# Optimization experiments

Measured on AMD Instinct MI355X. Metric: run time of the kernel, lower is better.

The kernel has to match this reference:

```python
import jax, jax.numpy as jnp
import numpy as np

BIN_SIZE = 128
DIST_MULT = 0.1
CLIP_LOW = 0.0
LN_EPS = 1e-6


def setup_inputs() -> dict:
    key = jax.random.key(0)
    ks = jax.random.split(key, 16)
    B, N, F = 8, 12800, 256
    D, H = 128, 256          # distance_dim, hidden_dim
    MAX_BINS = 200
    s = lambda k, shape: jax.random.normal(k, shape, dtype=jnp.float32) * 0.05
    return {
        "x": jax.random.normal(ks[0], (B, N, F), dtype=jnp.float32),
        "msk": jnp.ones((B, N), dtype=bool),
        "rotations": jax.random.normal(ks[1], (D, MAX_BINS // 2), dtype=jnp.float32),
        "ln_gamma": jnp.ones((F,), dtype=jnp.float32),
        "ln_beta": jnp.zeros((F,), dtype=jnp.float32),
        "w0": s(ks[2], (F, H)), "b0": jnp.zeros((H,), jnp.float32),
        "w1": s(ks[3], (H, H)), "b1": jnp.zeros((H,), jnp.float32),
        "w2": s(ks[4], (H, D)), "b2": jnp.zeros((D,), jnp.float32),
        "W_t": s(ks[5], (F, F)), "b_t": jnp.zeros((F,), jnp.float32),
        "W_h": s(ks[6], (F, F)),
        "theta": s(ks[7], (F, F)),
    }


def _forward(x, msk, rotations, ln_gamma, ln_beta, w0, b0, w1, b1, w2, b2,
             W_t, b_t, W_h, theta):
    B, N, F = x.shape
    n_bins = N // BIN_SIZE

    # LayerNormalization(axis=-1, epsilon=1e-6)
    mu = jnp.mean(x, axis=-1, keepdims=True)
    var = jnp.var(x, axis=-1, keepdims=True)
    xn = (x - mu) * jax.lax.rsqrt(var + LN_EPS) * ln_gamma + ln_beta

    # ffn_dist: two elu hidden layers + linear output to distance_dim
    h = jax.nn.elu(xn @ w0 + b0)
    h = jax.nn.elu(h @ w1 + b1)
    x_dist = h @ w2 + b2                                   # [B, N, D]

    # LSH binning: project, argmax over signed projections, argsort into bins
    mul = x_dist @ rotations[:, : n_bins // 2]             # [B, N, n_bins/2]
    cmul = jnp.concatenate([mul, -mul], axis=-1)           # [B, N, n_bins]
    bin_idx = jnp.argmax(cmul, axis=-1) + jnp.where(~msk, n_bins - 1, 0)
    bins_split = jnp.argsort(bin_idx, axis=-1).reshape(B, n_bins, BIN_SIZE)
    flat = bins_split.reshape(B, N)

    def take(a):  # gather with batch_dims=1, then split into bins
        return jnp.take_along_axis(a, flat[..., None], axis=1).reshape(
            B, n_bins, BIN_SIZE, a.shape[-1])

    x_msg_b = take(x_dist)                                 # [B, nb, bs, D]
    x_feat_b = take(xn)                                    # [B, nb, bs, F]
    msk_b = take(msk.astype(x.dtype)[..., None])           # [B, nb, bs, 1]

    # NodePairGaussianKernel on each bin
    na = jnp.sum(x_msg_b * x_msg_b, axis=-1)               # [B, nb, bs]
    d2 = (na[..., :, None] - 2.0 * jnp.einsum('bnif,bnjf->bnij', x_msg_b, x_msg_b)
          + na[..., None, :])
    dm = jnp.exp(-DIST_MULT * jnp.sqrt(jnp.maximum(d2, 1e-6)))
    dm = jnp.clip(dm, CLIP_LOW, 1.0)
    m = msk_b[..., 0]
    dm = dm * m[..., :, None] * m[..., None, :]            # [B, nb, bs, bs]

    # GHConvDense message passing (normalize_degrees=True, elu)
    in_deg = jnp.clip(jnp.sum(jnp.abs(dm), axis=-1), 0.0, 1000.0)
    norm = ((in_deg + 1e-6) ** -0.5)[..., None] * msk_b    # [B, nb, bs, 1]
    xm = x_feat_b * msk_b
    f_hom = (xm @ theta) * msk_b
    f_hom = jnp.einsum('bnij,bnjf->bnif', dm, f_hom * norm) * norm
    f_het = xm @ W_h
    gate = jax.nn.sigmoid(x_feat_b @ W_t + b_t)
    out = jax.nn.elu(gate * f_hom + (1.0 - gate) * f_het) * msk_b

    # reverse_lsh: scatter binned points back to original order
    pts = out.reshape(B, N, F)
    enc = jnp.zeros_like(pts).at[jnp.arange(B)[:, None], flat].set(pts)
    return enc


def reference(x, msk, rotations, ln_gamma, ln_beta, w0, b0, w1, b1, w2, b2,
              W_t, b_t, W_h, theta):
    return _forward(x, msk, rotations, ln_gamma, ln_beta, w0, b0, w1, b1,
                    w2, b2, W_t, b_t, W_h, theta)
```

## Files before the change

### kernel.cpp

```cpp
#include <hip/hip_runtime.h>


#define Bc   8
#define Nc   12800
#define Fc   256
#define Dc   128
#define NBINS 100
#define NBH  50
#define NPB  64
#define SPLT2 16384
#define TIE_TAU 1.0e-3f
#define FLAG_CAP 16384
#define WS_NEED 133062784ULL

typedef __attribute__((ext_vector_type(8))) short short8v;
typedef __attribute__((ext_vector_type(8))) _Float16 half8v;
typedef __attribute__((ext_vector_type(4))) _Float16 half4v;
typedef __attribute__((ext_vector_type(4))) float f32x4;

__device__ __forceinline__ float eluf(float v) { return v > 0.f ? v : __expf(v) - 1.f; }
__device__ __forceinline__ unsigned short f2bf(float f) {
  unsigned u = __float_as_uint(f);
  unsigned r = (u + 0x7FFFu + ((u >> 16) & 1u)) >> 16;
  return (unsigned short)r;
}
__device__ __forceinline__ float bf2f(unsigned short h) {
  return __uint_as_float((unsigned)h << 16);
}
__device__ __forceinline__ void split2(float v, _Float16 h[2]) {
  h[0] = (_Float16)v;
  h[1] = (_Float16)((v - (float)h[0]) * 2048.f);
}
#define C1 (1.f/2048.f)

__global__ void k0_prep(const float* __restrict__ theta, const float* __restrict__ Wh,
                        const float* __restrict__ Wt, const float* __restrict__ w0,
                        const float* __restrict__ w1, const float* __restrict__ w2,
                        const float* __restrict__ rot,
                        unsigned short* __restrict__ wcat, _Float16* __restrict__ w0s,
                        _Float16* __restrict__ w1s, _Float16* __restrict__ w2s,
                        _Float16* __restrict__ rots, int* __restrict__ flag_cnt)
{
  const int k = blockIdx.x, n = threadIdx.x;
  if (k == 0 && n == 0) *flag_cnt = 0;
  for (int nn = n; nn < 768; nn += 256) {
    const int sel = nn >> 8, f = nn & 255;
    const float* W = sel == 0 ? theta : (sel == 1 ? Wh : Wt);
    wcat[(size_t)nn*256 + k] = f2bf(W[k*256 + f]);
  }
  _Float16 h[2];
  split2(w0[k*256 + n], h);
#pragma unroll
  for (int s = 0; s < 2; ++s) w0s[s*65536 + n*256 + k] = h[s];
  split2(w1[k*256 + n], h);
#pragma unroll
  for (int s = 0; s < 2; ++s) w1s[s*65536 + n*256 + k] = h[s];
  if (n < 128) {
    split2(w2[k*128 + n], h);
#pragma unroll
    for (int s = 0; s < 2; ++s) w2s[s*32768 + n*256 + k] = h[s];
  }
  if (k < 128 && n < 112) {
    const float v = (n < NBINS) ? rot[k*100 + n] : 0.f;
    split2(v, h);
#pragma unroll
    for (int s = 0; s < 2; ++s) rots[s*14336 + n*128 + k] = h[s];
  }
}

template<int RT, int NT, int KS, int NSTR>
__device__ __forceinline__ void gemm3(const _Float16* __restrict__ sAb,
    const _Float16* __restrict__ B, int ldb, int bsplit, int n0, int lr, int lk,
    f32x4 aM[RT][NT], f32x4 aC1[RT][NT])
{
#pragma unroll
  for (int ks = 0; ks < KS; ++ks) {
    half8v a[2][RT], b[2][NT];
#pragma unroll
    for (int s = 0; s < 2; ++s) {
#pragma unroll
      for (int rt = 0; rt < RT; ++rt)
        a[s][rt] = *(const half8v*)&sAb[s*SPLT2 + (ks*4 + lk)*(NPB*8) + (rt*16 + lr)*8];
#pragma unroll
      for (int nt = 0; nt < NT; ++nt)
        b[s][nt] = *(const half8v*)&B[s*bsplit + (n0 + nt*NSTR + lr)*ldb + ks*32 + lk*8];
    }
#pragma unroll
    for (int rt = 0; rt < RT; ++rt)
#pragma unroll
      for (int nt = 0; nt < NT; ++nt) {
        aM[rt][nt]  = __builtin_amdgcn_mfma_f32_16x16x32_f16(a[0][rt], b[0][nt], aM[rt][nt], 0,0,0);
        aC1[rt][nt] = __builtin_amdgcn_mfma_f32_16x16x32_f16(a[0][rt], b[1][nt], aC1[rt][nt],0,0,0);
        aC1[rt][nt] = __builtin_amdgcn_mfma_f32_16x16x32_f16(a[1][rt], b[0][nt], aC1[rt][nt],0,0,0);
      }
  }
}

__global__ __launch_bounds__(512, 2) void k1_mfma(
    const float* __restrict__ x, const float* __restrict__ gamma, const float* __restrict__ beta,
    const _Float16* __restrict__ w0s, const _Float16* __restrict__ w1s,
    const _Float16* __restrict__ w2s, const _Float16* __restrict__ rots,
    const float* __restrict__ b0, const float* __restrict__ b1, const float* __restrict__ b2,
    unsigned short* __restrict__ xn_out, unsigned short* __restrict__ xd_out,
    int* __restrict__ bin_out, int* __restrict__ flag_cnt, int* __restrict__ flag_list)
{
  __shared__ __align__(16) _Float16 sA4[2*SPLT2];

  const int t = threadIdx.x;
  const int w = t >> 6, l = t & 63;
  const int lr = l & 15, lk = l >> 4;
  const int pt0 = blockIdx.x * NPB;

  {
    const int r = t >> 3, c8 = t & 7;
    const float* xr = x + (size_t)(pt0 + r)*Fc + c8*32;
    float4 xv[8];
    float s1 = 0.f, s2 = 0.f;
#pragma unroll
    for (int i = 0; i < 8; ++i) {
      xv[i] = *(const float4*)&xr[i*4];
      s1 += xv[i].x + xv[i].y + xv[i].z + xv[i].w;
      s2 += xv[i].x*xv[i].x + xv[i].y*xv[i].y + xv[i].z*xv[i].z + xv[i].w*xv[i].w;
    }
    s1 += __shfl_xor(s1, 1); s2 += __shfl_xor(s2, 1);
    s1 += __shfl_xor(s1, 2); s2 += __shfl_xor(s2, 2);
    s1 += __shfl_xor(s1, 4); s2 += __shfl_xor(s2, 4);
    const float mu = s1 * (1.f/256.f);
    const float var = s2 * (1.f/256.f) - mu*mu;
    const float rs = 1.f / sqrtf(var + 1e-6f);
#pragma unroll
    for (int i = 0; i < 8; ++i) {
      const int c = c8*32 + i*4;
      const float4 g  = *(const float4*)&gamma[c];
      const float4 be = *(const float4*)&beta[c];
      float v[4] = { (xv[i].x-mu)*rs*g.x + be.x, (xv[i].y-mu)*rs*g.y + be.y,
                     (xv[i].z-mu)*rs*g.z + be.z, (xv[i].w-mu)*rs*g.w + be.w };
      ushort4 ov; _Float16 h[4][2];
#pragma unroll
      for (int e = 0; e < 4; ++e) split2(v[e], h[e]);
      ov.x = f2bf(v[0]); ov.y = f2bf(v[1]); ov.z = f2bf(v[2]); ov.w = f2bf(v[3]);
      *(ushort4*)&xn_out[(size_t)(pt0 + r)*Fc + c] = ov;
      const int off = (c >> 3)*(NPB*8) + r*8 + (c & 7);
#pragma unroll
      for (int s = 0; s < 2; ++s) {
        half4v hv; hv[0]=h[0][s]; hv[1]=h[1][s]; hv[2]=h[2][s]; hv[3]=h[3][s];
        *(half4v*)&sA4[s*SPLT2 + off] = hv;
      }
    }
  }
  __syncthreads();

#pragma unroll 1
  for (int layer = 0; layer < 2; ++layer) {
    const _Float16* Bw = layer ? w1s : w0s;
    const float*    bb = layer ? b1  : b0;
    f32x4 aM[4][2], aC1[4][2];
#pragma unroll
    for (int rt = 0; rt < 4; ++rt)
#pragma unroll
      for (int nt = 0; nt < 2; ++nt) {
        aM[rt][nt] = (f32x4){0,0,0,0}; aC1[rt][nt] = (f32x4){0,0,0,0};
      }
    gemm3<4,2,8,16>(sA4, Bw, 256, 65536, w*32, lr, lk, aM, aC1);
    float vals[4][2][4];
#pragma unroll
    for (int nt = 0; nt < 2; ++nt) {
      const float bias = bb[w*32 + nt*16 + lr];
#pragma unroll
      for (int rt = 0; rt < 4; ++rt)
#pragma unroll
        for (int rr = 0; rr < 4; ++rr)
          vals[rt][nt][rr] = eluf(aM[rt][nt][rr] + aC1[rt][nt][rr]*C1 + bias);
    }
    __syncthreads();
#pragma unroll
    for (int nt = 0; nt < 2; ++nt) {
      const int col = w*32 + nt*16 + lr;
      const int base = (col >> 3)*(NPB*8) + (col & 7);
#pragma unroll
      for (int rt = 0; rt < 4; ++rt)
#pragma unroll
        for (int rr = 0; rr < 4; ++rr) {
          const int row = rt*16 + lk*4 + rr;
          _Float16 h[2]; split2(vals[rt][nt][rr], h);
          const int off = base + row*8;
          sA4[off] = h[0]; sA4[SPLT2 + off] = h[1];
        }
    }
    __syncthreads();
  }

  {
    f32x4 aM[4][1], aC1[4][1];
#pragma unroll
    for (int rt = 0; rt < 4; ++rt) { aM[rt][0] = (f32x4){0,0,0,0}; aC1[rt][0] = (f32x4){0,0,0,0}; }
    gemm3<4,1,8,16>(sA4, w2s, 256, 32768, w*16, lr, lk, aM, aC1);
    float vals[4][4];
    const int col = w*16 + lr;
    const float bias = b2[col];
#pragma unroll
    for (int rt = 0; rt < 4; ++rt)
#pragma unroll
      for (int rr = 0; rr < 4; ++rr) {
        const float v = aM[rt][0][rr] + aC1[rt][0][rr]*C1 + bias;
        vals[rt][rr] = v;
        xd_out[(size_t)(pt0 + rt*16 + lk*4 + rr)*Dc + col] = f2bf(v);
      }
    __syncthreads();
    {
      const int base = (col >> 3)*(NPB*8) + (col & 7);
#pragma unroll
      for (int rt = 0; rt < 4; ++rt)
#pragma unroll
        for (int rr = 0; rr < 4; ++rr) {
          const int row = rt*16 + lk*4 + rr;
          _Float16 h[2]; split2(vals[rt][rr], h);
          const int off = base + row*8;
          sA4[off] = h[0]; sA4[SPLT2 + off] = h[1];
        }
    }
    __syncthreads();
  }

  {
    float pv[4][4];
    if (w < 7) {
      f32x4 aM[4][1], aC1[4][1];
#pragma unroll
      for (int rt = 0; rt < 4; ++rt) { aM[rt][0] = (f32x4){0,0,0,0}; aC1[rt][0] = (f32x4){0,0,0,0}; }
      gemm3<4,1,4,16>(sA4, rots, 128, 14336, w*16, lr, lk, aM, aC1);
#pragma unroll
      for (int rt = 0; rt < 4; ++rt)
#pragma unroll
        for (int rr = 0; rr < 4; ++rr)
          pv[rt][rr] = aM[rt][0][rr] + aC1[rt][0][rr]*C1;
    }
    float* sMul = (float*)sA4;
    __syncthreads();
    if (w < 7) {
#pragma unroll
      for (int rt = 0; rt < 4; ++rt)
#pragma unroll
        for (int rr = 0; rr < 4; ++rr)
          sMul[(rt*16 + lk*4 + rr)*116 + w*16 + lr] = pv[rt][rr];
    }
    __syncthreads();
    if (t < NPB) {
      float best = -3.0e38f, second = -3.0e38f; int bi = 0;
      for (int j = 0; j < NBINS; ++j) {
        const float v = (j < NBH) ? sMul[t*116 + j] : -sMul[t*116 + (j - NBH)];
        if (v > best) { second = best; best = v; bi = j; }
        else if (v > second) second = v;
      }
      bin_out[pt0 + t] = bi;
      if (best - second < TIE_TAU) {
        const int slot = atomicAdd(flag_cnt, 1);
        if (slot < FLAG_CAP) flag_list[slot] = pt0 + t;
      }
    }
  }
}

__global__ __launch_bounds__(256) void k1b_repair(
    const float* __restrict__ x, const float* __restrict__ gamma, const float* __restrict__ beta,
    const float* __restrict__ w0, const float* __restrict__ b0,
    const float* __restrict__ w1, const float* __restrict__ b1,
    const float* __restrict__ w2, const float* __restrict__ b2,
    const float* __restrict__ rot,
    const int* __restrict__ flag_cnt, const int* __restrict__ flag_list,
    int* __restrict__ bin_out)
{
  const int n = min(*flag_cnt, FLAG_CAP);
  __shared__ float s0[256], s1[256], rs1[4], rs2[4];
  const int t = threadIdx.x;

  for (int it = blockIdx.x; it < n; it += gridDim.x) {
    const int p = flag_list[it];
    const float xv = x[(size_t)p*Fc + t];
    float a1 = xv, a2 = xv*xv;
#pragma unroll
    for (int o = 1; o < 64; o <<= 1) { a1 += __shfl_xor(a1, o); a2 += __shfl_xor(a2, o); }
    if ((t & 63) == 0) { rs1[t>>6] = a1; rs2[t>>6] = a2; }
    __syncthreads();
    const float S1 = rs1[0]+rs1[1]+rs1[2]+rs1[3];
    const float S2 = rs2[0]+rs2[1]+rs2[2]+rs2[3];
    const float mu = S1 * (1.f/256.f);
    const float var = S2 * (1.f/256.f) - mu*mu;
    const float rsv = 1.f / sqrtf(var + 1e-6f);
    s0[t] = (xv - mu) * rsv * gamma[t] + beta[t];
    __syncthreads();
    float acc = 0.f;
    for (int k = 0; k < 256; ++k) acc += s0[k] * w0[k*256 + t];
    const float h0v = eluf(acc + b0[t]);
    __syncthreads(); s1[t] = h0v; __syncthreads();
    acc = 0.f;
    for (int k = 0; k < 256; ++k) acc += s1[k] * w1[k*256 + t];
    const float h1v = eluf(acc + b1[t]);
    __syncthreads(); s0[t] = h1v; __syncthreads();
    if (t < 128) {
      acc = 0.f;
      for (int k = 0; k < 256; ++k) acc += s0[k] * w2[k*128 + t];
      s1[t] = acc + b2[t];
    }
    __syncthreads();
    if (t < NBINS) {
      float m = 0.f;
      for (int d = 0; d < 128; ++d) m += s1[d] * rot[d*100 + t];
      s0[t] = m;
    }
    __syncthreads();
    if (t == 0) {
      float best = -3.0e38f; int bi = 0;
      for (int j = 0; j < NBINS; ++j) {
        const float v = (j < NBH) ? s0[j] : -s0[j - NBH];
        if (v > best) { best = v; bi = j; }
      }
      bin_out[p] = bi;
    }
    __syncthreads();
  }
}

__global__ __launch_bounds__(256) void k2_sort(const int* __restrict__ bin_idx,
                                               int* __restrict__ flat)
{
  __shared__ unsigned int hist[NBINS][256];
  __shared__ unsigned int off[NBINS];
  const int b = blockIdx.x, t = threadIdx.x;
  for (int i = t; i < NBINS*256; i += 256) ((unsigned int*)hist)[i] = 0u;
  __syncthreads();
  const int* bi = bin_idx + b*Nc;
  const int start = t * 50;
  for (int i = 0; i < 50; ++i) hist[bi[start+i]][t]++;
  __syncthreads();
  for (int bb = t; bb < NBINS; bb += 256) {
    unsigned run = 0;
    for (int q = 0; q < 256; ++q) { const unsigned v = hist[bb][q]; hist[bb][q] = run; run += v; }
    off[bb] = run;
  }
  __syncthreads();
  if (t == 0) {
    unsigned run = 0;
    for (int q = 0; q < NBINS; ++q) { const unsigned v = off[q]; off[q] = run; run += v; }
  }
  __syncthreads();
  int* fo = flat + b*Nc;
  for (int i = 0; i < 50; ++i) {
    const int idx = start + i;
    const int bb = bi[idx];
    fo[off[bb] + hist[bb][t]++] = idx;
  }
}

__global__ __launch_bounds__(256) void k1g_hg(
    const unsigned short* __restrict__ xn, const unsigned short* __restrict__ wcat,
    const float* __restrict__ bt, float* __restrict__ out,
    unsigned short* __restrict__ gatebuf)
{
  __shared__ __align__(16) unsigned short sX[32*256];
  const int t = threadIdx.x;
  const int w = t >> 6, l = t & 63;
  const int lr = l & 15, lk = l >> 4;
  const int pt0 = blockIdx.x * 32;

  {
    const int r = t >> 3, c8 = t & 7;
    const unsigned short* src = xn + (size_t)(pt0 + r)*Fc + c8*32;
#pragma unroll
    for (int i = 0; i < 4; ++i) {
      const int c = c8*32 + i*8;
      *(short8v*)&sX[(c >> 3)*256 + r*8] = *(const short8v*)(src + i*8);
    }
  }
  __syncthreads();

#pragma unroll 1
  for (int cs = 0; cs < 4; ++cs) {
    const int f0 = w*64 + cs*16;
    f32x4 hacc[2], gacc[2];
#pragma unroll
    for (int rt = 0; rt < 2; ++rt) { hacc[rt] = (f32x4){0,0,0,0}; gacc[rt] = (f32x4){0,0,0,0}; }
    const unsigned short* bh = wcat + (size_t)(256 + f0 + lr)*256 + lk*8;
    const unsigned short* bg = wcat + (size_t)(512 + f0 + lr)*256 + lk*8;
#pragma unroll
    for (int ks = 0; ks < 8; ++ks) {
      short8v a0 = *(const short8v*)&sX[(ks*4 + lk)*256 + (lr)*8];
      short8v a1 = *(const short8v*)&sX[(ks*4 + lk)*256 + (16 + lr)*8];
      short8v bhv = *(const short8v*)(bh + ks*32);
      short8v bgv = *(const short8v*)(bg + ks*32);
      hacc[0] = __builtin_amdgcn_mfma_f32_16x16x32_bf16(a0, bhv, hacc[0], 0, 0, 0);
      hacc[1] = __builtin_amdgcn_mfma_f32_16x16x32_bf16(a1, bhv, hacc[1], 0, 0, 0);
      gacc[0] = __builtin_amdgcn_mfma_f32_16x16x32_bf16(a0, bgv, gacc[0], 0, 0, 0);
      gacc[1] = __builtin_amdgcn_mfma_f32_16x16x32_bf16(a1, bgv, gacc[1], 0, 0, 0);
    }
    const int f = f0 + lr;
    const float btf = bt[f];
#pragma unroll
    for (int rt = 0; rt < 2; ++rt)
#pragma unroll
      for (int rr = 0; rr < 4; ++rr) {
        const int p = pt0 + rt*16 + lk*4 + rr;
        const float g = 1.f / (1.f + __expf(-(gacc[rt][rr] + btf)));
        out[(size_t)p*Fc + f] = (1.f - g) * hacc[rt][rr];
        gatebuf[(size_t)p*Fc + f] = f2bf(g);
      }
  }
}

#define SXD 136

__global__ __launch_bounds__(512, 2) void k3_hoist(
    const unsigned short* __restrict__ xn, const unsigned short* __restrict__ xd,
    const int* __restrict__ flat, const unsigned short* __restrict__ wcat,
    const unsigned short* __restrict__ gatebuf, float* __restrict__ out)
{
  __shared__ __align__(16) unsigned short s_xd[128*SXD];
  __shared__ __align__(16) unsigned short s_dm[128*SXD];
  __shared__ __align__(16) unsigned short s_gt[32*SXD];
  __shared__ int   s_idx[128];
  __shared__ float s_na[128];
  __shared__ float s_norm[128];

  const int t = threadIdx.x;
  const int l = t & 63, w = t >> 6;
  const int lr = l & 15, lk = l >> 4;
  const int b = blockIdx.x / NBINS, bin = blockIdx.x % NBINS;
  const int base = b * Nc;

  if (t < 128) s_idx[t] = flat[base + bin*128 + t];
  __syncthreads();

  {
    const int r0 = t >> 4, c = t & 15;
    for (int r = r0; r < 128; r += 32) {
      const unsigned short* src = xd + (size_t)(base + s_idx[r])*Dc + c*8;
      *(short8v*)&s_xd[r*SXD + c*8] = *(const short8v*)src;
    }
  }
  __syncthreads();
  if (t < 128) {
    float s = 0.f;
    for (int c = 0; c < 16; ++c) {
      short8v v = *(short8v*)&s_xd[t*SXD + c*8];
#pragma unroll
      for (int e = 0; e < 8; ++e) { const float f = bf2f((unsigned short)v[e]); s += f*f; }
    }
    s_na[t] = s;
  }
  __syncthreads();

  {
    short8v a[4];
    const int arow = w*16 + lr;
#pragma unroll
    for (int kg = 0; kg < 4; ++kg)
      a[kg] = *(short8v*)&s_xd[arow*SXD + kg*32 + lk*8];
#pragma unroll 1
    for (int tj = 0; tj < 8; ++tj) {
      const int brow = tj*16 + lr;
      f32x4 acc = {0.f, 0.f, 0.f, 0.f};
#pragma unroll
      for (int kg = 0; kg < 4; ++kg) {
        short8v bv = *(short8v*)&s_xd[brow*SXD + kg*32 + lk*8];
        acc = __builtin_amdgcn_mfma_f32_16x16x32_bf16(a[kg], bv, acc, 0, 0, 0);
      }
      const int jj = tj*16 + lr;
      const float naj = s_na[jj];
#pragma unroll
      for (int r = 0; r < 4; ++r) {
        const int ii = w*16 + lk*4 + r;
        const float d2 = s_na[ii] + naj - 2.f*acc[r];
        s_dm[ii*SXD + jj] = f2bf(__expf(-0.1f * sqrtf(fmaxf(d2, 1e-6f))));
      }
    }
  }
  __syncthreads();
  if (t < 128) {
    float s = 0.f;
    for (int c = 0; c < 16; ++c) {
      short8v v = *(short8v*)&s_dm[t*SXD + c*8];
#pragma unroll
      for (int e = 0; e < 8; ++e) s += bf2f((unsigned short)v[e]);
    }
    s = fminf(fmaxf(s, 0.f), 1000.f);
    s_norm[t] = 1.f / sqrtf(s + 1e-6f);
  }
  __syncthreads();

  const size_t xrow = (size_t)(base + s_idx[w*16 + lr]) * Fc;

#pragma unroll 1
  for (int ch = 0; ch < 8; ++ch) {
    const int f0 = ch * 32;
    short8v A[8];
#pragma unroll
    for (int kg = 0; kg < 8; ++kg)
      A[kg] = *(const short8v*)&xn[xrow + kg*32 + lk*8];
#pragma unroll
    for (int tf = 0; tf < 2; ++tf) {
      const int f = f0 + tf*16 + lr;
      const unsigned short* bp = wcat + (size_t)f*256 + lk*8;
      f32x4 tacc = {0.f,0.f,0.f,0.f};
#pragma unroll
      for (int kg = 0; kg < 8; ++kg) {
        short8v bv = *(const short8v*)(bp + kg*32);
        tacc = __builtin_amdgcn_mfma_f32_16x16x32_bf16(A[kg], bv, tacc, 0, 0, 0);
      }
#pragma unroll
      for (int r = 0; r < 4; ++r) {
        const int j = w*16 + lk*4 + r;
        s_gt[(tf*16 + lr)*SXD + j] = f2bf(tacc[r] * s_norm[j]);
      }
    }
    __syncthreads();
    {
      const int irow = w*16 + lr;
#pragma unroll
      for (int tf = 0; tf < 2; ++tf) {
        const int f = f0 + tf*16 + lr;
        f32x4 facc = {0.f, 0.f, 0.f, 0.f};
#pragma unroll
        for (int kg = 0; kg < 4; ++kg) {
          short8v ad  = *(short8v*)&s_dm[irow*SXD + kg*32 + lk*8];
          short8v bgt = *(short8v*)&s_gt[(tf*16 + lr)*SXD + kg*32 + lk*8];
          facc = __builtin_amdgcn_mfma_f32_16x16x32_bf16(ad, bgt, facc, 0, 0, 0);
        }
#pragma unroll
        for (int r = 0; r < 4; ++r) {
          const int i = w*16 + lk*4 + r;
          const size_t orow = (size_t)(base + s_idx[i]) * Fc + f;
          const float fh = facc[r] * s_norm[i];
          const float g  = bf2f(gatebuf[orow]);
          const float partial = out[orow];
          out[orow] = eluf(g * fh + partial);
        }
      }
    }
    __syncthreads();
  }
}

__global__ __launch_bounds__(512, 2) void k3_bins(
    const unsigned short* __restrict__ xn, const unsigned short* __restrict__ xd,
    const int* __restrict__ flat, const unsigned short* __restrict__ wcat,
    const float* __restrict__ bt, float* __restrict__ out)
{
  __shared__ __align__(16) unsigned short s_buf[128*SXD];
  __shared__ __align__(16) unsigned short s_gt[32*SXD];
  __shared__ int   s_idx[128];
  __shared__ float s_na[128];
  __shared__ float s_norm[128];

  const int t = threadIdx.x;
  const int l = t & 63, w = t >> 6;
  const int lr = l & 15, lk = l >> 4;
  const int b = blockIdx.x / NBINS, bin = blockIdx.x % NBINS;
  const int base = b * Nc;

  if (t < 128) s_idx[t] = flat[base + bin*128 + t];
  __syncthreads();
  {
    const int r0 = t >> 4, c = t & 15;
    for (int r = r0; r < 128; r += 32) {
      const unsigned short* src = xd + (size_t)(base + s_idx[r])*Dc + c*8;
      *(short8v*)&s_buf[r*SXD + c*8] = *(const short8v*)src;
    }
  }
  __syncthreads();
  if (t < 128) {
    float s = 0.f;
    for (int c = 0; c < 16; ++c) {
      short8v v = *(short8v*)&s_buf[t*SXD + c*8];
#pragma unroll
      for (int e = 0; e < 8; ++e) { const float f = bf2f((unsigned short)v[e]); s += f*f; }
    }
    s_na[t] = s;
  }
  __syncthreads();
  {
    f32x4 dot[8];
    short8v a[4];
    const int arow = w*16 + lr;
#pragma unroll
    for (int kg = 0; kg < 4; ++kg)
      a[kg] = *(short8v*)&s_buf[arow*SXD + kg*32 + lk*8];
#pragma unroll
    for (int tj = 0; tj < 8; ++tj) {
      const int brow = tj*16 + lr;
      f32x4 acc = {0.f, 0.f, 0.f, 0.f};
#pragma unroll
      for (int kg = 0; kg < 4; ++kg) {
        short8v bv = *(short8v*)&s_buf[brow*SXD + kg*32 + lk*8];
        acc = __builtin_amdgcn_mfma_f32_16x16x32_bf16(a[kg], bv, acc, 0, 0, 0);
      }
      dot[tj] = acc;
    }
    __syncthreads();
#pragma unroll
    for (int tj = 0; tj < 8; ++tj) {
      const int jj = tj*16 + lr;
      const float naj = s_na[jj];
#pragma unroll
      for (int r = 0; r < 4; ++r) {
        const int ii = w*16 + lk*4 + r;
        const float d2 = s_na[ii] + naj - 2.f*dot[tj][r];
        s_buf[ii*SXD + jj] = f2bf(__expf(-0.1f * sqrtf(fmaxf(d2, 1e-6f))));
      }
    }
  }
  __syncthreads();
  if (t < 128) {
    float s = 0.f;
    for (int c = 0; c < 16; ++c) {
      short8v v = *(short8v*)&s_buf[t*SXD + c*8];
#pragma unroll
      for (int e = 0; e < 8; ++e) s += bf2f((unsigned short)v[e]);
    }
    s = fminf(fmaxf(s, 0.f), 1000.f);
    s_norm[t] = 1.f / sqrtf(s + 1e-6f);
  }
  __syncthreads();

  const size_t xrow = (size_t)(base + s_idx[w*16 + lr]) * Fc;
#pragma unroll 1
  for (int ch = 0; ch < 8; ++ch) {
    const int f0 = ch * 32;
    float hg_h[2][4], hg_g[2][4];
    short8v A[8];
#pragma unroll
    for (int kg = 0; kg < 8; ++kg)
      A[kg] = *(const short8v*)&xn[xrow + kg*32 + lk*8];
#pragma unroll
    for (int tf = 0; tf < 2; ++tf) {
      const int f = f0 + tf*16 + lr;
      const unsigned short* bp = wcat + (size_t)f*256 + lk*8;
      const unsigned short* bh = wcat + (size_t)(256 + f)*256 + lk*8;
      const unsigned short* bg = wcat + (size_t)(512 + f)*256 + lk*8;
      f32x4 tacc = {0.f,0.f,0.f,0.f}, hacc = {0.f,0.f,0.f,0.f}, gacc = {0.f,0.f,0.f,0.f};
#pragma unroll
      for (int kg = 0; kg < 8; ++kg) {
        short8v bv = *(const short8v*)(bp + kg*32);
        tacc = __builtin_amdgcn_mfma_f32_16x16x32_bf16(A[kg], bv, tacc, 0, 0, 0);
        short8v hv = *(const short8v*)(bh + kg*32);
        hacc = __builtin_amdgcn_mfma_f32_16x16x32_bf16(A[kg], hv, hacc, 0, 0, 0);
        short8v gv = *(const short8v*)(bg + kg*32);
        gacc = __builtin_amdgcn_mfma_f32_16x16x32_bf16(A[kg], gv, gacc, 0, 0, 0);
      }
#pragma unroll
      for (int r = 0; r < 4; ++r) {
        const int j = w*16 + lk*4 + r;
        s_gt[(tf*16 + lr)*SXD + j] = f2bf(tacc[r] * s_norm[j]);
        hg_h[tf][r] = hacc[r];
        hg_g[tf][r] = gacc[r];
      }
    }
    __syncthreads();
    {
      const int irow = w*16 + lr;
#pragma unroll
      for (int tf = 0; tf < 2; ++tf) {
        const int f = f0 + tf*16 + lr;
        f32x4 facc = {0.f, 0.f, 0.f, 0.f};
#pragma unroll
        for (int kg = 0; kg < 4; ++kg) {
          short8v ad  = *(short8v*)&s_buf[irow*SXD + kg*32 + lk*8];
          short8v bgt = *(short8v*)&s_gt[(tf*16 + lr)*SXD + kg*32 + lk*8];
          facc = __builtin_amdgcn_mfma_f32_16x16x32_bf16(ad, bgt, facc, 0, 0, 0);
        }
        const float btf = bt[f];
#pragma unroll
        for (int r = 0; r < 4; ++r) {
          const int i = w*16 + lk*4 + r;
          const float fh = facc[r] * s_norm[i];
          const float g  = 1.f / (1.f + __expf(-(hg_g[tf][r] + btf)));
          const float val = g * fh + (1.f - g) * hg_h[tf][r];
          out[(size_t)(base + s_idx[i])*Fc + f] = eluf(val);
        }
      }
    }
    __syncthreads();
  }
}

extern "C" void kernel_launch(void* const* d_in, const int* in_sizes, int n_in,
                              void* d_out, int out_size, void* d_ws, size_t ws_size,
                              hipStream_t stream)
{
  const float* x     = (const float*)d_in[0];
  const float* rot   = (const float*)d_in[2];
  const float* gamma = (const float*)d_in[3];
  const float* beta  = (const float*)d_in[4];
  const float* w0    = (const float*)d_in[5];
  const float* b0    = (const float*)d_in[6];
  const float* w1    = (const float*)d_in[7];
  const float* b1    = (const float*)d_in[8];
  const float* w2    = (const float*)d_in[9];
  const float* b2    = (const float*)d_in[10];
  const float* Wt    = (const float*)d_in[11];
  const float* bt    = (const float*)d_in[12];
  const float* Wh    = (const float*)d_in[13];
  const float* theta = (const float*)d_in[14];
  float* out = (float*)d_out;

  char* ws = (char*)d_ws;
  unsigned short* xn   = (unsigned short*)ws;
  unsigned short* xd   = (unsigned short*)(ws + 52428800);
  int* binv            = (int*)(ws + 78643200);
  int* flat            = (int*)(ws + 79052800);
  unsigned short* wcat = (unsigned short*)(ws + 79462400);
  _Float16* w0s        = (_Float16*)(ws + 79855616);
  _Float16* w1s        = (_Float16*)(ws + 80117760);
  _Float16* w2s        = (_Float16*)(ws + 80379904);
  _Float16* rots       = (_Float16*)(ws + 80510976);
  int* fcnt            = (int*)(ws + 80568320);
  int* flist           = (int*)(ws + 80568448);
  unsigned short* gate = (unsigned short*)(ws + 80633984);

  const bool hoist = (ws_size >= WS_NEED);

  k0_prep<<<dim3(256), dim3(256), 0, stream>>>(theta, Wh, Wt, w0, w1, w2, rot,
                                               wcat, w0s, w1s, w2s, rots, fcnt);
  k1_mfma<<<dim3((Bc*Nc)/NPB), dim3(512), 0, stream>>>(
      x, gamma, beta, w0s, w1s, w2s, rots, b0, b1, b2, xn, xd, binv, fcnt, flist);
  k1b_repair<<<dim3(2048), dim3(256), 0, stream>>>(
      x, gamma, beta, w0, b0, w1, b1, w2, b2, rot, fcnt, flist, binv);
  k2_sort<<<dim3(Bc), dim3(256), 0, stream>>>(binv, flat);
  if (hoist) {
    k1g_hg<<<dim3((Bc*Nc)/32), dim3(256), 0, stream>>>(xn, wcat, bt, out, gate);
    k3_hoist<<<dim3(Bc*NBINS), dim3(512), 0, stream>>>(
        xn, xd, flat, wcat, gate, out);
  } else {
    k3_bins<<<dim3(Bc*NBINS), dim3(512), 0, stream>>>(
        xn, xd, flat, wcat, bt, out);
  }
}
```

Baseline: 578.3 us.

## Hoist theta projection into unbinned gate/het kernel, store bf16 intermediate

```diff
diff --git a/kernel.cpp b/kernel.cpp
--- a/kernel.cpp
+++ b/kernel.cpp
@@ -11,7 +11,8 @@
 #define SPLT2 16384
 #define TIE_TAU 1.0e-3f
 #define FLAG_CAP 16384
-#define WS_NEED 133062784ULL
+#define WS_NEED1 133062784ULL
+#define WS_NEED2 185491584ULL
 
 typedef __attribute__((ext_vector_type(8))) short short8v;
 typedef __attribute__((ext_vector_type(8))) _Float16 half8v;
@@ -352,6 +353,68 @@
   }
 }
 
+__global__ __launch_bounds__(256) void k1g_hg3(
+    const unsigned short* __restrict__ xn, const unsigned short* __restrict__ wcat,
+    const float* __restrict__ bt, float* __restrict__ out,
+    unsigned short* __restrict__ gatebuf, unsigned short* __restrict__ gtall)
+{
+  __shared__ __align__(16) unsigned short sX[32*256];
+  const int t = threadIdx.x;
+  const int w = t >> 6, l = t & 63;
+  const int lr = l & 15, lk = l >> 4;
+  const int pt0 = blockIdx.x * 32;
+
+  {
+    const int r = t >> 3, c8 = t & 7;
+    const unsigned short* src = xn + (size_t)(pt0 + r)*Fc + c8*32;
+#pragma unroll
+    for (int i = 0; i < 4; ++i) {
+      const int c = c8*32 + i*8;
+      *(short8v*)&sX[(c >> 3)*256 + r*8] = *(const short8v*)(src + i*8);
+    }
+  }
+  __syncthreads();
+
+#pragma unroll 1
+  for (int cs = 0; cs < 4; ++cs) {
+    const int f0 = w*64 + cs*16;
+    f32x4 hacc[2], gacc[2], tacc[2];
+#pragma unroll
+    for (int rt = 0; rt < 2; ++rt) {
+      hacc[rt] = (f32x4){0,0,0,0}; gacc[rt] = (f32x4){0,0,0,0}; tacc[rt] = (f32x4){0,0,0,0};
+    }
+    const unsigned short* bp = wcat + (size_t)(f0 + lr)*256 + lk*8;
+    const unsigned short* bh = wcat + (size_t)(256 + f0 + lr)*256 + lk*8;
+    const unsigned short* bg = wcat + (size_t)(512 + f0 + lr)*256 + lk*8;
+#pragma unroll
+    for (int ks = 0; ks < 8; ++ks) {
+      short8v a0 = *(const short8v*)&sX[(ks*4 + lk)*256 + (lr)*8];
+      short8v a1 = *(const short8v*)&sX[(ks*4 + lk)*256 + (16 + lr)*8];
+      short8v btv = *(const short8v*)(bp + ks*32);
+      short8v bhv = *(const short8v*)(bh + ks*32);
+      short8v bgv = *(const short8v*)(bg + ks*32);
+      tacc[0] = __builtin_amdgcn_mfma_f32_16x16x32_bf16(a0, btv, tacc[0], 0, 0, 0);
+      tacc[1] = __builtin_amdgcn_mfma_f32_16x16x32_bf16(a1, btv, tacc[1], 0, 0, 0);
+      hacc[0] = __builtin_amdgcn_mfma_f32_16x16x32_bf16(a0, bhv, hacc[0], 0, 0, 0);
+      hacc[1] = __builtin_amdgcn_mfma_f32_16x16x32_bf16(a1, bhv, hacc[1], 0, 0, 0);
+      gacc[0] = __builtin_amdgcn_mfma_f32_16x16x32_bf16(a0, bgv, gacc[0], 0, 0, 0);
+      gacc[1] = __builtin_amdgcn_mfma_f32_16x16x32_bf16(a1, bgv, gacc[1], 0, 0, 0);
+    }
+    const int f = f0 + lr;
+    const float btf = bt[f];
+#pragma unroll
+    for (int rt = 0; rt < 2; ++rt)
+#pragma unroll
+      for (int rr = 0; rr < 4; ++rr) {
+        const int p = pt0 + rt*16 + lk*4 + rr;
+        const float g = 1.f / (1.f + __expf(-(gacc[rt][rr] + btf)));
+        out[(size_t)p*Fc + f] = (1.f - g) * hacc[rt][rr];
+        gatebuf[(size_t)p*Fc + f] = f2bf(g);
+        gtall[(size_t)p*Fc + f] = f2bf(tacc[rt][rr]);
+      }
+  }
+}
+
 __global__ __launch_bounds__(256) void k1g_hg(
     const unsigned short* __restrict__ xn, const unsigned short* __restrict__ wcat,
     const float* __restrict__ bt, float* __restrict__ out,
@@ -409,9 +472,9 @@
 
 #define SXD 136
 
-__global__ __launch_bounds__(512, 2) void k3_hoist(
-    const unsigned short* __restrict__ xn, const unsigned short* __restrict__ xd,
-    const int* __restrict__ flat, const unsigned short* __restrict__ wcat,
+__global__ __launch_bounds__(512, 2) void k3_hoist2(
+    const unsigned short* __restrict__ xd, const int* __restrict__ flat,
+    const unsigned short* __restrict__ gtall,
     const unsigned short* __restrict__ gatebuf, float* __restrict__ out)
 {
   __shared__ __align__(16) unsigned short s_xd[128*SXD];
@@ -487,8 +550,122 @@
   }
   __syncthreads();
 
+#pragma unroll 1
+  for (int ch = 0; ch < 8; ++ch) {
+    const int f0 = ch * 32;
+    {
+      const int r = t >> 2, cc = (t & 3) * 8;
+      short8v v = *(const short8v*)&gtall[(size_t)(base + s_idx[r])*Fc + f0 + cc];
+      const float nr = s_norm[r];
+#pragma unroll
+      for (int e = 0; e < 8; ++e)
+        s_gt[(cc + e)*SXD + r] = f2bf(bf2f((unsigned short)v[e]) * nr);
+    }
+    __syncthreads();
+    {
+      const int irow = w*16 + lr;
+#pragma unroll
+      for (int tf = 0; tf < 2; ++tf) {
+        const int f = f0 + tf*16 + lr;
+        f32x4 facc = {0.f, 0.f, 0.f, 0.f};
+#pragma unroll
+        for (int kg = 0; kg < 4; ++kg) {
+          short8v ad  = *(short8v*)&s_dm[irow*SXD + kg*32 + lk*8];
+          short8v bgt = *(short8v*)&s_gt[(tf*16 + lr)*SXD + kg*32 + lk*8];
+          facc = __builtin_amdgcn_mfma_f32_16x16x32_bf16(ad, bgt, facc, 0, 0, 0);
+        }
+#pragma unroll
+        for (int r = 0; r < 4; ++r) {
+          const int i = w*16 + lk*4 + r;
+          const size_t orow = (size_t)(base + s_idx[i]) * Fc + f;
+          const float fh = facc[r] * s_norm[i];
+          const float g  = bf2f(gatebuf[orow]);
+          const float partial = out[orow];
+          out[orow] = eluf(g * fh + partial);
+        }
+      }
+    }
+    __syncthreads();
+  }
+}
+
+__global__ __launch_bounds__(512, 2) void k3_hoist(
+    const unsigned short* __restrict__ xn, const unsigned short* __restrict__ xd,
+    const int* __restrict__ flat, const unsigned short* __restrict__ wcat,
+    const unsigned short* __restrict__ gatebuf, float* __restrict__ out)
+{
+  __shared__ __align__(16) unsigned short s_xd[128*SXD];
+  __shared__ __align__(16) unsigned short s_dm[128*SXD];
+  __shared__ __align__(16) unsigned short s_gt[32*SXD];
+  __shared__ int   s_idx[128];
+  __shared__ float s_na[128];
+  __shared__ float s_norm[128];
+
+  const int t = threadIdx.x;
+  const int l = t & 63, w = t >> 6;
+  const int lr = l & 15, lk = l >> 4;
+  const int b = blockIdx.x / NBINS, bin = blockIdx.x % NBINS;
+  const int base = b * Nc;
+
+  if (t < 128) s_idx[t] = flat[base + bin*128 + t];
+  __syncthreads();
+  {
+    const int r0 = t >> 4, c = t & 15;
+    for (int r = r0; r < 128; r += 32) {
+      const unsigned short* src = xd + (size_t)(base + s_idx[r])*Dc + c*8;
+      *(short8v*)&s_xd[r*SXD + c*8] = *(const short8v*)src;
+    }
+  }
+  __syncthreads();
+  if (t < 128) {
+    float s = 0.f;
+    for (int c = 0; c < 16; ++c) {
+      short8v v = *(short8v*)&s_xd[t*SXD + c*8];
+#pragma unroll
+      for (int e = 0; e < 8; ++e) { const float f = bf2f((unsigned short)v[e]); s += f*f; }
+    }
+    s_na[t] = s;
+  }
+  __syncthreads();
+  {
+    short8v a[4];
+    const int arow = w*16 + lr;
+#pragma unroll
+    for (int kg = 0; kg < 4; ++kg)
+      a[kg] = *(short8v*)&s_xd[arow*SXD + kg*32 + lk*8];
+#pragma unroll 1
+    for (int tj = 0; tj < 8; ++tj) {
+      const int brow = tj*16 + lr;
+      f32x4 acc = {0.f, 0.f, 0.f, 0.f};
+#pragma unroll
+      for (int kg = 0; kg < 4; ++kg) {
+        short8v bv = *(short8v*)&s_xd[brow*SXD + kg*32 + lk*8];
+        acc = __builtin_amdgcn_mfma_f32_16x16x32_bf16(a[kg], bv, acc, 0, 0, 0);
+      }
+      const int jj = tj*16 + lr;
+      const float naj = s_na[jj];
+#pragma unroll
+      for (int r = 0; r < 4; ++r) {
+        const int ii = w*16 + lk*4 + r;
+        const float d2 = s_na[ii] + naj - 2.f*acc[r];
+        s_dm[ii*SXD + jj] = f2bf(__expf(-0.1f * sqrtf(fmaxf(d2, 1e-6f))));
+      }
+    }
+  }
+  __syncthreads();
+  if (t < 128) {
+    float s = 0.f;
+    for (int c = 0; c < 16; ++c) {
+      short8v v = *(short8v*)&s_dm[t*SXD + c*8];
+#pragma unroll
+      for (int e = 0; e < 8; ++e) s += bf2f((unsigned short)v[e]);
+    }
+    s = fminf(fmaxf(s, 0.f), 1000.f);
+    s_norm[t] = 1.f / sqrtf(s + 1e-6f);
+  }
+  __syncthreads();
+
   const size_t xrow = (size_t)(base + s_idx[w*16 + lr]) * Fc;
-
 #pragma unroll 1
   for (int ch = 0; ch < 8; ++ch) {
     const int f0 = ch * 32;
@@ -703,20 +880,21 @@
   float* out = (float*)d_out;
 
   char* ws = (char*)d_ws;
-  unsigned short* xn   = (unsigned short*)ws;
-  unsigned short* xd   = (unsigned short*)(ws + 52428800);
-  int* binv            = (int*)(ws + 78643200);
-  int* flat            = (int*)(ws + 79052800);
-  unsigned short* wcat = (unsigned short*)(ws + 79462400);
-  _Float16* w0s        = (_Float16*)(ws + 79855616);
-  _Float16* w1s        = (_Float16*)(ws + 80117760);
-  _Float16* w2s        = (_Float16*)(ws + 80379904);
-  _Float16* rots       = (_Float16*)(ws + 80510976);
-  int* fcnt            = (int*)(ws + 80568320);
-  int* flist           = (int*)(ws + 80568448);
-  unsigned short* gate = (unsigned short*)(ws + 80633984);
-
-  const bool hoist = (ws_size >= WS_NEED);
+  unsigned short* xn    = (unsigned short*)ws;
+  unsigned short* xd    = (unsigned short*)(ws + 52428800);
+  int* binv             = (int*)(ws + 78643200);
+  int* flat             = (int*)(ws + 79052800);
+  unsigned short* wcat  = (unsigned short*)(ws + 79462400);
+  _Float16* w0s         = (_Float16*)(ws + 79855616);
+  _Float16* w1s         = (_Float16*)(ws + 80117760);
+  _Float16* w2s         = (_Float16*)(ws + 80379904);
+  _Float16* rots        = (_Float16*)(ws + 80510976);
+  int* fcnt             = (int*)(ws + 80568320);
+  int* flist            = (int*)(ws + 80568448);
+  unsigned short* gate  = (unsigned short*)(ws + 80633984);
+  unsigned short* gtall = (unsigned short*)(ws + 133062784);
+
+  const int lvl = (ws_size >= WS_NEED2) ? 2 : (ws_size >= WS_NEED1) ? 1 : 0;
 
   k0_prep<<<dim3(256), dim3(256), 0, stream>>>(theta, Wh, Wt, w0, w1, w2, rot,
                                                wcat, w0s, w1s, w2s, rots, fcnt);
@@ -725,12 +903,13 @@
   k1b_repair<<<dim3(2048), dim3(256), 0, stream>>>(
       x, gamma, beta, w0, b0, w1, b1, w2, b2, rot, fcnt, flist, binv);
   k2_sort<<<dim3(Bc), dim3(256), 0, stream>>>(binv, flat);
-  if (hoist) {
+  if (lvl == 2) {
+    k1g_hg3<<<dim3((Bc*Nc)/32), dim3(256), 0, stream>>>(xn, wcat, bt, out, gate, gtall);
+    k3_hoist2<<<dim3(Bc*NBINS), dim3(512), 0, stream>>>(xd, flat, gtall, gate, out);
+  } else if (lvl == 1) {
     k1g_hg<<<dim3((Bc*Nc)/32), dim3(256), 0, stream>>>(xn, wcat, bt, out, gate);
-    k3_hoist<<<dim3(Bc*NBINS), dim3(512), 0, stream>>>(
-        xn, xd, flat, wcat, gate, out);
+    k3_hoist<<<dim3(Bc*NBINS), dim3(512), 0, stream>>>(xn, xd, flat, wcat, gate, out);
   } else {
-    k3_bins<<<dim3(Bc*NBINS), dim3(512), 0, stream>>>(
-        xn, xd, flat, wcat, bt, out);
-  }
-}
+    k3_bins<<<dim3(Bc*NBINS), dim3(512), 0, stream>>>(xn, xd, flat, wcat, bt, out);
+  }
+}
```

New measurement: 596.3 us. 1.03x slower.
